# Performance work log

Measured on AMD Instinct MI355X. Metric: run time of the kernel, lower is better.

Reference implementation:

```python
import jax, jax.numpy as jnp
import numpy as np

EPS = 1e-5

def layernorm(x, w, b):
    mu = jnp.mean(x, axis=-1, keepdims=True)
    xc = x - mu
    var = jnp.mean(xc * xc, axis=-1, keepdims=True)
    return xc * jax.lax.rsqrt(var + EPS) * w + b

def setup_inputs() -> dict:
    key = jax.random.key(0)
    ks = jax.random.split(key, 9)
    B, T, Nm, Nl = 8, 8, 1024, 64
    Vw, Tw, H, Dh = 1024, 2048, 8, 64
    inner = H * Dh  # 512
    s_q = 1.0 / np.sqrt(Tw)
    s_kv = 1.0 / np.sqrt(Vw)
    s_o = 1.0 / np.sqrt(inner)
    return {
        "x": jax.random.normal(ks[0], (B, T, Nm, Vw), jnp.float32),
        "latents": jax.random.normal(ks[1], (B, T, Nl, Tw), jnp.float32),
        "nm_w": jnp.ones((Vw,), jnp.float32),
        "nm_b": jnp.zeros((Vw,), jnp.float32),
        "nl_w": jnp.ones((Tw,), jnp.float32),
        "nl_b": jnp.zeros((Tw,), jnp.float32),
        "Wq": jax.random.normal(ks[2], (Tw, inner), jnp.float32) * s_q,
        "Wkv": jax.random.normal(ks[3], (Vw, 2 * inner), jnp.float32) * s_kv,
        "Wout": jax.random.normal(ks[4], (inner, Tw), jnp.float32) * s_o,
    }

def reference(x, latents, nm_w, nm_b, nl_w, nl_b, Wq, Wkv, Wout):
    H, Dh = 8, 64
    scale = Dh ** (-0.5)
    B, T, Nm, _ = x.shape
    Nl = latents.shape[2]
    xn = layernorm(x, nm_w, nm_b)          # (B,T,Nm,Vw)
    ln = layernorm(latents, nl_w, nl_b)    # (B,T,Nl,Tw)
    q = (ln @ Wq).reshape(B, T, Nl, H, Dh)           # b t i h d
    kv = xn @ Wkv                                     # (B,T,Nm,2*inner)
    k, v = jnp.split(kv, 2, axis=-1)
    k = k.reshape(B, T, Nm, H, Dh)                    # b t j h d
    v = v.reshape(B, T, Nm, H, Dh)
    sim = jnp.einsum('btihd,btjhd->bthij', q * scale, k)  # (B,T,H,Nl,Nm)
    attn = jax.nn.softmax(sim, axis=-1)
    out = jnp.einsum('bthij,btjhd->btihd', attn, v)       # (B,T,Nl,H,Dh)
    out = out.reshape(B, T, Nl, H * Dh)
    return out @ Wout                                     # (B,T,Nl,Tw)
```

## Files before the change

kernel.cpp:

```cpp
#include <hip/hip_runtime.h>

typedef __attribute__((ext_vector_type(8))) short bfrag8;
typedef __attribute__((ext_vector_type(4))) float f32x4;

typedef const unsigned int __attribute__((address_space(1)))* gas1_u32;
typedef unsigned int __attribute__((address_space(3)))* gas3_u32;

#define DEV __device__ __forceinline__

DEV unsigned short f2bf(float f) {
  unsigned int u = __builtin_bit_cast(unsigned int, f);
  u += 0x7fffu + ((u >> 16) & 1u);
  return (unsigned short)(u >> 16);
}

DEV void gload_lds16(const void* g, void* l) {
  __builtin_amdgcn_global_load_lds((gas1_u32)g, (gas3_u32)l, 16, 0, 0);
}

__global__ __launch_bounds__(256) void k_xstats(
    const float* __restrict__ x, unsigned short* __restrict__ xb,
    float* __restrict__ mu, float* __restrict__ rstd)
{
  const int wid = threadIdx.x >> 6, lane = threadIdx.x & 63;
  const int row = blockIdx.x * 4 + wid;
  const float* base = x + (size_t)row * 1024;
  float4 v[4];
  #pragma unroll
  for (int i = 0; i < 4; ++i) v[i] = ((const float4*)base)[i * 64 + lane];
  float s = 0.f, q = 0.f;
  #pragma unroll
  for (int i = 0; i < 4; ++i) {
    s += v[i].x + v[i].y + v[i].z + v[i].w;
    q += v[i].x*v[i].x + v[i].y*v[i].y + v[i].z*v[i].z + v[i].w*v[i].w;
  }
  #pragma unroll
  for (int off = 32; off >= 1; off >>= 1) { s += __shfl_xor(s, off); q += __shfl_xor(q, off); }
  const float m  = s * (1.0f/1024.0f);
  const float var = q * (1.0f/1024.0f) - m * m;
  const float rs = rsqrtf(var + 1e-5f);
  if (lane == 0) { mu[row] = m; rstd[row] = rs; }
  unsigned short* ob = xb + (size_t)row * 1024;
  #pragma unroll
  for (int i = 0; i < 4; ++i) {
    ushort4 o;
    o.x = f2bf(v[i].x); o.y = f2bf(v[i].y); o.z = f2bf(v[i].z); o.w = f2bf(v[i].w);
    ((ushort4*)ob)[i * 64 + lane] = o;
  }
}

__global__ __launch_bounds__(256) void k_lnlat(
    const float* __restrict__ lat, const float* __restrict__ w,
    const float* __restrict__ b, unsigned short* __restrict__ ln)
{
  const int row = blockIdx.x, tid = threadIdx.x;
  const float* base = lat + (size_t)row * 2048;
  const float4 v0 = ((const float4*)base)[tid];
  const float4 v1 = ((const float4*)base)[256 + tid];
  float s = v0.x+v0.y+v0.z+v0.w + v1.x+v1.y+v1.z+v1.w;
  float q = v0.x*v0.x+v0.y*v0.y+v0.z*v0.z+v0.w*v0.w
          + v1.x*v1.x+v1.y*v1.y+v1.z*v1.z+v1.w*v1.w;
  #pragma unroll
  for (int off = 32; off >= 1; off >>= 1) { s += __shfl_xor(s, off); q += __shfl_xor(q, off); }
  __shared__ float red[8];
  const int wid = tid >> 6, lane = tid & 63;
  if (lane == 0) { red[wid] = s; red[4 + wid] = q; }
  __syncthreads();
  s = red[0] + red[1] + red[2] + red[3];
  q = red[4] + red[5] + red[6] + red[7];
  const float m  = s * (1.0f/2048.0f);
  const float var = q * (1.0f/2048.0f) - m * m;
  const float rs = rsqrtf(var + 1e-5f);
  const float4 w0 = ((const float4*)w)[tid], w1 = ((const float4*)w)[256 + tid];
  const float4 b0 = ((const float4*)b)[tid], b1 = ((const float4*)b)[256 + tid];
  ushort4 o0, o1;
  o0.x = f2bf((v0.x - m) * rs * w0.x + b0.x);
  o0.y = f2bf((v0.y - m) * rs * w0.y + b0.y);
  o0.z = f2bf((v0.z - m) * rs * w0.z + b0.z);
  o0.w = f2bf((v0.w - m) * rs * w0.w + b0.w);
  o1.x = f2bf((v1.x - m) * rs * w1.x + b1.x);
  o1.y = f2bf((v1.y - m) * rs * w1.y + b1.y);
  o1.z = f2bf((v1.z - m) * rs * w1.z + b1.z);
  o1.w = f2bf((v1.w - m) * rs * w1.w + b1.w);
  ((ushort4*)(ln + (size_t)row * 2048))[tid] = o0;
  ((ushort4*)(ln + (size_t)row * 2048))[256 + tid] = o1;
}

__global__ __launch_bounds__(256) void k_transpose_cast(
    const float* __restrict__ src, unsigned short* __restrict__ dst,
    int K, int N, const float* __restrict__ rowscale, float scale)
{
  __shared__ float tile[32][33];
  const int tx = threadIdx.x & 31, ty = threadIdx.x >> 5;
  const int ntiles = N >> 5;
  const int k0 = (blockIdx.x / ntiles) << 5;
  const int n0 = (blockIdx.x % ntiles) << 5;
  #pragma unroll
  for (int r = 0; r < 4; ++r) {
    const int kk = ty + r * 8;
    float v = src[(size_t)(k0 + kk) * N + n0 + tx] * scale;
    if (rowscale) v *= rowscale[k0 + kk];
    tile[kk][tx] = v;
  }
  __syncthreads();
  #pragma unroll
  for (int r = 0; r < 4; ++r) {
    const int nn = ty + r * 8;
    dst[(size_t)(n0 + nn) * K + k0 + tx] = f2bf(tile[tx][nn]);
  }
}

__global__ __launch_bounds__(256) void k_c1c2_part(
    const float* __restrict__ Wkv, const float* __restrict__ w,
    const float* __restrict__ b, float* __restrict__ part)
{
  const int kc = blockIdx.x;
  const int n  = blockIdx.y * 256 + threadIdx.x;
  float s1 = 0.f, s2 = 0.f;
  const int k0 = kc * 64;
  for (int k = k0; k < k0 + 64; ++k) {
    const float wv = Wkv[(size_t)k * 1024 + n];
    s1 += w[k] * wv;
    s2 += b[k] * wv;
  }
  part[(size_t)(kc * 2 + 0) * 1024 + n] = s1;
  part[(size_t)(kc * 2 + 1) * 1024 + n] = s2;
}

__global__ __launch_bounds__(256) void k_c1c2_red(
    const float* __restrict__ part, float* __restrict__ c1, float* __restrict__ c2)
{
  const int n = blockIdx.x * 256 + threadIdx.x;
  float s1 = 0.f, s2 = 0.f;
  #pragma unroll
  for (int kc = 0; kc < 16; ++kc) {
    s1 += part[(size_t)(kc * 2 + 0) * 1024 + n];
    s2 += part[(size_t)(kc * 2 + 1) * 1024 + n];
  }
  c1[n] = s1; c2[n] = s2;
}

template<int BM, int BN, int WM, int WN, int NT, int MODE>
__global__ __launch_bounds__(NT, 2) void k_gemm(
    const unsigned short* __restrict__ A, int lda,
    const unsigned short* __restrict__ Bt, int ldb,
    int K, int mtiles, int ntiles,
    void* __restrict__ Cout, int ldc,
    const float* __restrict__ mu, const float* __restrict__ rstd,
    const float* __restrict__ c1, const float* __restrict__ c2)
{
  constexpr int BK = 32;
  constexpr int NW = NT / 64;
  constexpr int MF = (BM / WM) / 16;
  constexpr int NF = (BN / WN) / 16;
  constexpr int LA = (BM * BK) / (8 * NT);
  constexpr int LB = (BN * BK) / (8 * NT);
  constexpr int RA = BM * BK;
  constexpr int RB = BN * BK;
  static_assert(WM * WN == NW, "wave grid");
  static_assert(LA >= 1 && LB >= 1, "tile too small for NT");

  __shared__ __attribute__((aligned(16))) unsigned short As[4 * RA];
  __shared__ __attribute__((aligned(16))) unsigned short Bs[4 * RB];

  int bid = blockIdx.x;
  {
    const int nwg = gridDim.x;
    if ((nwg & 7) == 0) {
      const int q = nwg >> 3;
      bid = (bid & 7) * q + (bid >> 3);
    }
  }
  const int mt = bid / ntiles, nt = bid % ntiles;
  const int tid = threadIdx.x;
  const int wid = tid >> 6, lane = tid & 63;
  const int g = lane >> 4, c = lane & 15;
  const int wr = wid / WN, wc = wid % WN;
  const int MO = wr * (BM / WM), NO = wc * (BN / WN);
  const int rot = (c >> 1) & 3;

  const unsigned short* gA = A + (size_t)mt * BM * lda;
  const unsigned short* gB = Bt + (size_t)nt * BN * ldb;

  const f32x4 zz = {0.f, 0.f, 0.f, 0.f};
  f32x4 acc[MF][NF];
  #pragma unroll
  for (int m = 0; m < MF; ++m)
    #pragma unroll
    for (int n = 0; n < NF; ++n) acc[m][n] = zz;

  auto stage = [&](int R, int kt) {
    #pragma unroll
    for (int i = 0; i < LA; ++i) {
      const int o = (i * NT + tid) * 16;
      const int row = o >> 6;
      const int slot = (o >> 4) & 3;
      const int srcb = (((slot - ((row >> 1) & 3)) & 3) << 4);
      gload_lds16((const char*)(gA + (size_t)row * lda + kt * BK) + srcb,
                  (char*)(As + R * RA) + o);
    }
    #pragma unroll
    for (int i = 0; i < LB; ++i) {
      const int o = (i * NT + tid) * 16;
      const int row = o >> 6;
      const int slot = (o >> 4) & 3;
      const int srcb = (((slot - ((row >> 1) & 3)) & 3) << 4);
      gload_lds16((const char*)(gB + (size_t)row * ldb + kt * BK) + srcb,
                  (char*)(Bs + R * RB) + o);
    }
  };

  auto compute = [&](int R) {
    const char* as = (const char*)(As + R * RA);
    const char* bs = (const char*)(Bs + R * RB);
    bfrag8 af[MF], bf[NF];
    #pragma unroll
    for (int m = 0; m < MF; ++m) {
      const int rw = MO + m * 16 + c;
      af[m] = *(const bfrag8*)(as + rw * 64 + (((g + rot) & 3) << 4));
    }
    #pragma unroll
    for (int n = 0; n < NF; ++n) {
      const int rw = NO + n * 16 + c;
      bf[n] = *(const bfrag8*)(bs + rw * 64 + (((g + rot) & 3) << 4));
    }
    #pragma unroll
    for (int m = 0; m < MF; ++m)
      #pragma unroll
      for (int n = 0; n < NF; ++n)
        acc[m][n] = __builtin_amdgcn_mfma_f32_16x16x32_bf16(af[m], bf[n], acc[m][n], 0, 0, 0);
  };

  const int nkt = K / BK;
  stage(0, 0); stage(1, 1); stage(2, 2);
  for (int t = 0; t < nkt; t += 4) {
    #pragma unroll
    for (int r = 0; r < 4; ++r) {
      int t3 = t + r + 3; if (t3 >= nkt) t3 -= nkt;
      asm volatile("s_waitcnt vmcnt(8)\n\ts_barrier" ::: "memory");
      stage((r + 3) & 3, t3);
      compute(r);
    }
  }

  #pragma unroll
  for (int m = 0; m < MF; ++m) {
    #pragma unroll
    for (int j = 0; j < 4; ++j) {
      const size_t orow = (size_t)mt * BM + MO + m * 16 + g * 4 + j;
      float rs = 0.f, muv = 0.f;
      if constexpr (MODE == 0) { rs = rstd[orow]; muv = mu[orow]; }
      #pragma unroll
      for (int n = 0; n < NF; ++n) {
        const int gcol = nt * BN + NO + n * 16 + c;
        float v = acc[m][n][j];
        if constexpr (MODE == 0) v = rs * (v - muv * c1[gcol]) + c2[gcol];
        if constexpr (MODE == 2) ((float*)Cout)[orow * ldc + gcol] = v;
        else ((unsigned short*)Cout)[orow * ldc + gcol] = f2bf(v);
      }
    }
  }
}

__global__ __launch_bounds__(256) void k_attn(
    const unsigned short* __restrict__ q,
    const unsigned short* __restrict__ kv,
    unsigned short* __restrict__ ao)
{
  __shared__ __attribute__((aligned(16))) unsigned short Vt[64 * 64];
  const int bid = blockIdx.x;
  const int bt = bid >> 3, h = bid & 7;
  const int tid = threadIdx.x;
  const int wid = tid >> 6, lane = tid & 63;
  const int g = lane >> 4, c = lane & 15;

  const size_t qoff = ((size_t)bt * 64 + wid * 16 + c) * 512 + h * 64;
  const bfrag8 qf0 = *(const bfrag8*)(q + qoff + g * 8);
  const bfrag8 qf1 = *(const bfrag8*)(q + qoff + 32 + g * 8);

  const f32x4 zz = {0.f, 0.f, 0.f, 0.f};
  f32x4 o[4] = {zz, zz, zz, zz};
  float m_run = -1e30f, l_run = 0.f;

  const size_t kvbase = (size_t)bt * 1024 * 1024;
  const unsigned short* kbase = kv + kvbase + h * 64;
  const unsigned short* vbase = kv + kvbase + 512 + h * 64;

  for (int ch = 0; ch < 16; ++ch) {
    #pragma unroll
    for (int rr = 0; rr < 2; ++rr) {
      const int key = rr * 32 + (tid >> 3);
      const int d0 = (tid & 7) * 8;
      const bfrag8 vv = *(const bfrag8*)(vbase + (size_t)(ch * 64 + key) * 1024 + d0);
      #pragma unroll
      for (int j = 0; j < 8; ++j)
        Vt[(d0 + j) * 64 + (key ^ (j << 3))] = (unsigned short)vv[j];
    }
    __syncthreads();
    #pragma unroll
    for (int ks = 0; ks < 2; ++ks) {
      const int kb = ch * 64 + ks * 32;
      f32x4 s[2];
      #pragma unroll
      for (int t = 0; t < 2; ++t) {
        const int kr = ((c >> 2) << 3) + (t << 2) + (c & 3);
        const unsigned short* krow = kbase + (size_t)(kb + kr) * 1024;
        s[t] = zz;
        s[t] = __builtin_amdgcn_mfma_f32_16x16x32_bf16(*(const bfrag8*)(krow + g * 8),      qf0, s[t], 0, 0, 0);
        s[t] = __builtin_amdgcn_mfma_f32_16x16x32_bf16(*(const bfrag8*)(krow + 32 + g * 8), qf1, s[t], 0, 0, 0);
      }
      float pm = s[0][0];
      #pragma unroll
      for (int i = 1; i < 4; ++i) pm = fmaxf(pm, s[0][i]);
      #pragma unroll
      for (int i = 0; i < 4; ++i) pm = fmaxf(pm, s[1][i]);
      pm = fmaxf(pm, __shfl_xor(pm, 16));
      pm = fmaxf(pm, __shfl_xor(pm, 32));
      const float mn = fmaxf(m_run, pm);
      const float alpha = __expf(m_run - mn);
      float p[8];
      #pragma unroll
      for (int i = 0; i < 4; ++i) p[i]     = __expf(s[0][i] - mn);
      #pragma unroll
      for (int i = 0; i < 4; ++i) p[4 + i] = __expf(s[1][i] - mn);
      float ts = 0.f;
      #pragma unroll
      for (int i = 0; i < 8; ++i) ts += p[i];
      ts += __shfl_xor(ts, 16);
      ts += __shfl_xor(ts, 32);
      l_run = l_run * alpha + ts;
      m_run = mn;
      float ar[4];
      #pragma unroll
      for (int rj = 0; rj < 4; ++rj) ar[rj] = __shfl(alpha, g * 4 + rj);
      #pragma unroll
      for (int db = 0; db < 4; ++db)
        #pragma unroll
        for (int j = 0; j < 4; ++j) o[db][j] *= ar[j];
      bfrag8 pa;
      #pragma unroll
      for (int i = 0; i < 8; ++i) pa[i] = (short)f2bf(p[i]);
      #pragma unroll
      for (int db = 0; db < 4; ++db) {
        const int d = db * 16 + c;
        const bfrag8 vb = *(const bfrag8*)(Vt + d * 64 + ((ks * 32 + g * 8) ^ ((c & 7) << 3)));
        o[db] = __builtin_amdgcn_mfma_f32_16x16x32_bf16(pa, vb, o[db], 0, 0, 0);
      }
    }
    __syncthreads();
  }
  float lr[4];
  #pragma unroll
  for (int rj = 0; rj < 4; ++rj) lr[rj] = __shfl(l_run, g * 4 + rj);
  #pragma unroll
  for (int db = 0; db < 4; ++db)
    #pragma unroll
    for (int j = 0; j < 4; ++j) {
      const float val = o[db][j] / lr[j];
      ao[((size_t)bt * 64 + wid * 16 + g * 4 + j) * 512 + h * 64 + db * 16 + c] = f2bf(val);
    }
}

extern "C" void kernel_launch(void* const* d_in, const int* in_sizes, int n_in,
                              void* d_out, int out_size, void* d_ws, size_t ws_size,
                              hipStream_t stream)
{
  const float* x    = (const float*)d_in[0];
  const float* lat  = (const float*)d_in[1];
  const float* nm_w = (const float*)d_in[2];
  const float* nm_b = (const float*)d_in[3];
  const float* nl_w = (const float*)d_in[4];
  const float* nl_b = (const float*)d_in[5];
  const float* Wq   = (const float*)d_in[6];
  const float* Wkv  = (const float*)d_in[7];
  const float* Wout = (const float*)d_in[8];

  char* p = (char*)d_ws;
  auto take = [&](size_t bytes) { char* r = p; p += (bytes + 255) & ~(size_t)255; return r; };
  unsigned short* xb    = (unsigned short*)take(64ull * 1024 * 1024 * 2);
  unsigned short* kvb   = (unsigned short*)take(64ull * 1024 * 1024 * 2);
  unsigned short* lnb   = (unsigned short*)take(4096ull * 2048 * 2);
  unsigned short* qbuf  = (unsigned short*)take(4096ull * 512 * 2);
  unsigned short* aob   = (unsigned short*)take(4096ull * 512 * 2);
  unsigned short* WqT   = (unsigned short*)take(512ull * 2048 * 2);
  unsigned short* WkvT  = (unsigned short*)take(1024ull * 1024 * 2);
  unsigned short* WoutT = (unsigned short*)take(2048ull * 512 * 2);
  float* muv  = (float*)take(65536ull * 4);
  float* rsd  = (float*)take(65536ull * 4);
  float* c1   = (float*)take(1024 * 4);
  float* c2   = (float*)take(1024 * 4);
  float* part = (float*)take(32ull * 1024 * 4);
  if ((size_t)(p - (char*)d_ws) > ws_size) return;

  k_transpose_cast<<<dim3(64 * 16), 256, 0, stream>>>(Wq,   WqT,   2048,  512, nullptr, 0.125f);
  k_transpose_cast<<<dim3(32 * 32), 256, 0, stream>>>(Wkv,  WkvT,  1024, 1024, nm_w,    1.0f);
  k_transpose_cast<<<dim3(16 * 64), 256, 0, stream>>>(Wout, WoutT,  512, 2048, nullptr, 1.0f);
  k_c1c2_part<<<dim3(16, 4), 256, 0, stream>>>(Wkv, nm_w, nm_b, part);
  k_c1c2_red<<<dim3(4), 256, 0, stream>>>(part, c1, c2);
  k_xstats<<<dim3(16384), 256, 0, stream>>>(x, xb, muv, rsd);
  k_lnlat<<<dim3(4096), 256, 0, stream>>>(lat, nl_w, nl_b, lnb);

  k_gemm<256, 256, 2, 4, 512, 0><<<dim3(1024), 512, 0, stream>>>(
      xb, 1024, WkvT, 1024, 1024, 256, 4, kvb, 1024, muv, rsd, c1, c2);
  k_gemm<128, 128, 2, 2, 256, 1><<<dim3(128), 256, 0, stream>>>(
      lnb, 2048, WqT, 2048, 2048, 32, 4, qbuf, 512, nullptr, nullptr, nullptr, nullptr);

  k_attn<<<dim3(512), 256, 0, stream>>>(qbuf, kvb, aob);

  k_gemm<128, 128, 2, 2, 256, 2><<<dim3(512), 256, 0, stream>>>(
      aob, 512, WoutT, 512, 512, 32, 16, d_out, 2048, nullptr, nullptr, nullptr, nullptr);
}
```

Baseline: 388.9 us.

## Add dedicated 8-wave KV GEMM with interleaved staging and retile Q/out GEMMs

Replaces the generic KV projection GEMM with a specialized 256x256 kernel using 64-wide K tiles, double-buffered 128KB LDS, and fine-grained interleaving of async global-to-LDS loads with MFMA blocks under s_setprio. The goal is to hide load latency behind matrix math and cut barrier stalls in the dominant GEMM. Separately, the Q and output GEMMs move to 64x128 tiles so they launch more workgroups, and the generic kernel's vmcnt gate now tracks its actual load count per stage. Risks include using a full 128KB of LDS, which limits occupancy, and hand-tuned wait counts that must match the issued loads exactly.

```diff
diff --git a/kernel.cpp b/kernel.cpp
--- a/kernel.cpp
+++ b/kernel.cpp
@@ -17,6 +17,11 @@
 DEV void gload_lds16(const void* g, void* l) {
   __builtin_amdgcn_global_load_lds((gas1_u32)g, (gas3_u32)l, 16, 0, 0);
 }
+
+template<int N> DEV void gate_bar();
+template<> DEV void gate_bar<4>() { asm volatile("s_waitcnt vmcnt(4)\n\ts_barrier" ::: "memory"); }
+template<> DEV void gate_bar<6>() { asm volatile("s_waitcnt vmcnt(6)\n\ts_barrier" ::: "memory"); }
+template<> DEV void gate_bar<8>() { asm volatile("s_waitcnt vmcnt(8)\n\ts_barrier" ::: "memory"); }
 
 __global__ __launch_bounds__(256) void k_xstats(
     const float* __restrict__ x, unsigned short* __restrict__ xb,
@@ -140,14 +145,156 @@
   c1[n] = s1; c2[n] = s2;
 }
 
+#define BAR8   __builtin_amdgcn_s_barrier()
+#define GATE4  do { gate_bar<4>(); __builtin_amdgcn_sched_barrier(0); } while (0)
+#define LGKM0  do { asm volatile("s_waitcnt lgkmcnt(0)" ::: "memory"); \
+                    __builtin_amdgcn_sched_barrier(0); } while (0)
+
+__global__ __launch_bounds__(512, 2) void k_gemm8(
+    const unsigned short* __restrict__ A,
+    const unsigned short* __restrict__ Bt,
+    unsigned short* __restrict__ C,
+    const float* __restrict__ mu, const float* __restrict__ rstd,
+    const float* __restrict__ c1, const float* __restrict__ c2)
+{
+  constexpr int NKT = 16;
+  __shared__ __attribute__((aligned(16))) char lds[131072];
+
+  int bid = blockIdx.x;
+  { const int nwg = gridDim.x; const int q = nwg >> 3; bid = (bid & 7) * q + (bid >> 3); }
+  const int mt = bid >> 2, nt = bid & 3;
+  const int tid = threadIdx.x;
+  const int wid = tid >> 6, lane = tid & 63;
+  const int g = lane >> 4, c = lane & 15;
+  const int wr = wid >> 2, wc = wid & 3;
+  const int MO = wr * 128, NO = wc * 64;
+
+  const unsigned short* gA = A + (size_t)mt * 256 * 1024;
+  const unsigned short* gB = Bt + (size_t)nt * 256 * 1024;
+
+  const f32x4 zz = {0.f, 0.f, 0.f, 0.f};
+  f32x4 acc[8][4];
+  #pragma unroll
+  for (int m = 0; m < 8; ++m)
+    #pragma unroll
+    for (int n = 0; n < 4; ++n) acc[m][n] = zz;
+
+  auto stageA = [&](int buf, int kk, int kt) {
+    #pragma unroll
+    for (int i = 0; i < 2; ++i) {
+      const int o = (i * 512 + tid) * 16;
+      const int row = o >> 6;
+      const int ss = ((((o >> 4) & 3) - (row >> 1)) & 3);
+      gload_lds16((const char*)(gA + (size_t)row * 1024 + kt * 64 + kk * 32) + ss * 16,
+                  lds + buf * 32768 + kk * 16384 + o);
+    }
+  };
+  auto stageB = [&](int buf, int kk, int kt) {
+    #pragma unroll
+    for (int i = 0; i < 2; ++i) {
+      const int o = (i * 512 + tid) * 16;
+      const int row = o >> 6;
+      const int ss = ((((o >> 4) & 3) - (row >> 1)) & 3);
+      gload_lds16((const char*)(gB + (size_t)row * 1024 + kt * 64 + kk * 32) + ss * 16,
+                  lds + 65536 + buf * 32768 + kk * 16384 + o);
+    }
+  };
+  auto rdA = [&](int buf, int kk, int m) -> bfrag8 {
+    const int row = MO + m * 16 + c;
+    return *(const bfrag8*)(lds + buf * 32768 + kk * 16384 + row * 64
+                            + (((g + (row >> 1)) & 3) << 4));
+  };
+  auto rdB = [&](int buf, int kk, int n) -> bfrag8 {
+    const int row = NO + n * 16 + c;
+    return *(const bfrag8*)(lds + 65536 + buf * 32768 + kk * 16384 + row * 64
+                            + (((g + (row >> 1)) & 3) << 4));
+  };
+
+  bfrag8 a[8], b0[4], b1[4];
+
+  auto tile4 = [&](int buf, int sb, int ukt) {
+    #pragma unroll
+    for (int m = 0; m < 8; ++m) a[m] = rdA(buf, 0, m);
+    #pragma unroll
+    for (int n = 0; n < 4; ++n) b0[n] = rdB(buf, 0, n);
+    stageA(sb, 0, ukt);
+    BAR8; LGKM0;
+    __builtin_amdgcn_s_setprio(1);
+    #pragma unroll
+    for (int m = 0; m < 8; ++m) {
+      acc[m][0] = __builtin_amdgcn_mfma_f32_16x16x32_bf16(a[m], b0[0], acc[m][0], 0, 0, 0);
+      acc[m][1] = __builtin_amdgcn_mfma_f32_16x16x32_bf16(a[m], b0[1], acc[m][1], 0, 0, 0);
+    }
+    __builtin_amdgcn_s_setprio(0);
+    GATE4;
+    #pragma unroll
+    for (int n = 0; n < 4; ++n) b1[n] = rdB(buf, 1, n);
+    stageB(sb, 0, ukt);
+    BAR8; LGKM0;
+    __builtin_amdgcn_s_setprio(1);
+    #pragma unroll
+    for (int m = 0; m < 8; ++m) {
+      acc[m][2] = __builtin_amdgcn_mfma_f32_16x16x32_bf16(a[m], b0[2], acc[m][2], 0, 0, 0);
+      acc[m][3] = __builtin_amdgcn_mfma_f32_16x16x32_bf16(a[m], b0[3], acc[m][3], 0, 0, 0);
+    }
+    __builtin_amdgcn_s_setprio(0);
+    GATE4;
+    #pragma unroll
+    for (int m = 0; m < 8; ++m) a[m] = rdA(buf, 1, m);
+    stageB(sb, 1, ukt);
+    BAR8; LGKM0;
+    __builtin_amdgcn_s_setprio(1);
+    #pragma unroll
+    for (int m = 0; m < 8; ++m) {
+      acc[m][0] = __builtin_amdgcn_mfma_f32_16x16x32_bf16(a[m], b1[0], acc[m][0], 0, 0, 0);
+      acc[m][1] = __builtin_amdgcn_mfma_f32_16x16x32_bf16(a[m], b1[1], acc[m][1], 0, 0, 0);
+    }
+    __builtin_amdgcn_s_setprio(0);
+    BAR8;
+    stageA(sb, 1, ukt);
+    BAR8; LGKM0;
+    __builtin_amdgcn_s_setprio(1);
+    #pragma unroll
+    for (int m = 0; m < 8; ++m) {
+      acc[m][2] = __builtin_amdgcn_mfma_f32_16x16x32_bf16(a[m], b1[2], acc[m][2], 0, 0, 0);
+      acc[m][3] = __builtin_amdgcn_mfma_f32_16x16x32_bf16(a[m], b1[3], acc[m][3], 0, 0, 0);
+    }
+    __builtin_amdgcn_s_setprio(0);
+    GATE4;
+  };
+
+  stageA(0, 0, 0); stageB(0, 0, 0); stageB(0, 1, 0); stageA(0, 1, 0);
+  GATE4;
+
+  for (int t = 0; t < NKT; t += 2) {
+    const int u2 = (t + 2 < NKT) ? t + 2 : 0;
+    tile4(0, 1, t + 1);
+    tile4(1, 0, u2);
+  }
+  asm volatile("s_waitcnt vmcnt(0)" ::: "memory");
+
+  #pragma unroll
+  for (int m = 0; m < 8; ++m) {
+    #pragma unroll
+    for (int j = 0; j < 4; ++j) {
+      const size_t orow = (size_t)mt * 256 + MO + m * 16 + g * 4 + j;
+      const float rs = rstd[orow], muv = mu[orow];
+      #pragma unroll
+      for (int n = 0; n < 4; ++n) {
+        const int gcol = nt * 256 + NO + n * 16 + c;
+        const float v = rs * (acc[m][n][j] - muv * c1[gcol]) + c2[gcol];
+        C[orow * 1024 + gcol] = f2bf(v);
+      }
+    }
+  }
+}
+
 template<int BM, int BN, int WM, int WN, int NT, int MODE>
 __global__ __launch_bounds__(NT, 2) void k_gemm(
     const unsigned short* __restrict__ A, int lda,
     const unsigned short* __restrict__ Bt, int ldb,
     int K, int mtiles, int ntiles,
-    void* __restrict__ Cout, int ldc,
-    const float* __restrict__ mu, const float* __restrict__ rstd,
-    const float* __restrict__ c1, const float* __restrict__ c2)
+    void* __restrict__ Cout, int ldc)
 {
   constexpr int BK = 32;
   constexpr int NW = NT / 64;
@@ -155,10 +302,12 @@
   constexpr int NF = (BN / WN) / 16;
   constexpr int LA = (BM * BK) / (8 * NT);
   constexpr int LB = (BN * BK) / (8 * NT);
+  constexpr int LPS = LA + LB;
   constexpr int RA = BM * BK;
   constexpr int RB = BN * BK;
   static_assert(WM * WN == NW, "wave grid");
   static_assert(LA >= 1 && LB >= 1, "tile too small for NT");
+  static_assert(LPS == 3 || LPS == 4, "gate specialization");
 
   __shared__ __attribute__((aligned(16))) unsigned short As[4 * RA];
   __shared__ __attribute__((aligned(16))) unsigned short Bs[4 * RB];
@@ -237,24 +386,23 @@
     #pragma unroll
     for (int r = 0; r < 4; ++r) {
       int t3 = t + r + 3; if (t3 >= nkt) t3 -= nkt;
-      asm volatile("s_waitcnt vmcnt(8)\n\ts_barrier" ::: "memory");
+      gate_bar<2 * LPS>();
+      __builtin_amdgcn_sched_barrier(0);
       stage((r + 3) & 3, t3);
       compute(r);
     }
   }
+  asm volatile("s_waitcnt vmcnt(0)" ::: "memory");
 
   #pragma unroll
   for (int m = 0; m < MF; ++m) {
     #pragma unroll
     for (int j = 0; j < 4; ++j) {
       const size_t orow = (size_t)mt * BM + MO + m * 16 + g * 4 + j;
-      float rs = 0.f, muv = 0.f;
-      if constexpr (MODE == 0) { rs = rstd[orow]; muv = mu[orow]; }
       #pragma unroll
       for (int n = 0; n < NF; ++n) {
         const int gcol = nt * BN + NO + n * 16 + c;
-        float v = acc[m][n][j];
-        if constexpr (MODE == 0) v = rs * (v - muv * c1[gcol]) + c2[gcol];
+        const float v = acc[m][n][j];
         if constexpr (MODE == 2) ((float*)Cout)[orow * ldc + gcol] = v;
         else ((unsigned short*)Cout)[orow * ldc + gcol] = f2bf(v);
       }
@@ -400,13 +548,12 @@
   k_xstats<<<dim3(16384), 256, 0, stream>>>(x, xb, muv, rsd);
   k_lnlat<<<dim3(4096), 256, 0, stream>>>(lat, nl_w, nl_b, lnb);
 
-  k_gemm<256, 256, 2, 4, 512, 0><<<dim3(1024), 512, 0, stream>>>(
-      xb, 1024, WkvT, 1024, 1024, 256, 4, kvb, 1024, muv, rsd, c1, c2);
-  k_gemm<128, 128, 2, 2, 256, 1><<<dim3(128), 256, 0, stream>>>(
-      lnb, 2048, WqT, 2048, 2048, 32, 4, qbuf, 512, nullptr, nullptr, nullptr, nullptr);
+  k_gemm8<<<dim3(1024), 512, 0, stream>>>(xb, WkvT, kvb, muv, rsd, c1, c2);
+  k_gemm<64, 128, 1, 4, 256, 1><<<dim3(256), 256, 0, stream>>>(
+      lnb, 2048, WqT, 2048, 2048, 64, 4, qbuf, 512);
 
   k_attn<<<dim3(512), 256, 0, stream>>>(qbuf, kvb, aob);
 
-  k_gemm<128, 128, 2, 2, 256, 2><<<dim3(512), 256, 0, stream>>>(
-      aob, 512, WoutT, 512, 512, 32, 16, d_out, 2048, nullptr, nullptr, nullptr, nullptr);
-}
+  k_gemm<64, 128, 1, 4, 256, 2><<<dim3(1024), 256, 0, stream>>>(
+      aob, 512, WoutT, 512, 512, 64, 16, d_out, 2048);
+}
```

New measurement: 378.4 us. 2.7% less time.

## Add dedicated KV GEMM kernel with register-held B fragments and retune other GEMMs

Applied to the files above, without the earlier changes.

Replaces the large 256x256 KV projection GEMM with a new 128x128 kernel. Only A tiles are staged through LDS, in a swizzled double buffer, while B fragments are loaded straight from global memory into registers and the LayerNorm correction is fused into the epilogue. The Q and output projections switch to 64x128 tiles to launch more workgroups, and the pipeline wait count is specialized per tile config. This trades LDS traffic and barrier cost for more global-load pressure and register use.

```diff
diff --git a/kernel.cpp b/kernel.cpp
--- a/kernel.cpp
+++ b/kernel.cpp
@@ -16,6 +16,12 @@
 
 DEV void gload_lds16(const void* g, void* l) {
   __builtin_amdgcn_global_load_lds((gas1_u32)g, (gas3_u32)l, 16, 0, 0);
+}
+
+template<int N> DEV void gate_bar();
+template<> DEV void gate_bar<6>() { asm volatile("s_waitcnt vmcnt(6)\n\ts_barrier" ::: "memory"); }
+template<> DEV void gate_bar<8>() {
+  asm volatile("s_waitcnt lgkmcnt(0)\n\ts_waitcnt vmcnt(8)\n\ts_barrier" ::: "memory");
 }
 
 __global__ __launch_bounds__(256) void k_xstats(
@@ -140,14 +146,114 @@
   c1[n] = s1; c2[n] = s2;
 }
 
+__global__ __launch_bounds__(256, 2) void k_gbr(
+    const unsigned short* __restrict__ A,
+    const unsigned short* __restrict__ Bt,
+    unsigned short* __restrict__ C,
+    const float* __restrict__ mu, const float* __restrict__ rstd,
+    const float* __restrict__ c1, const float* __restrict__ c2)
+{
+  constexpr int NKT = 16;
+  __shared__ __attribute__((aligned(16))) unsigned short Al[2][128 * 64];
+
+  int bid = blockIdx.x;
+  { const int nwg = gridDim.x; const int q = nwg >> 3; bid = (bid & 7) * q + (bid >> 3); }
+  const int mt = bid >> 3, nt = bid & 7;
+  const int tid = threadIdx.x;
+  const int wid = tid >> 6, lane = tid & 63;
+  const int g = lane >> 4, c = lane & 15;
+  const int wr = wid >> 1, wc = wid & 1;
+  const int MO = wr * 64, NO = wc * 64;
+
+  const unsigned short* gA = A + (size_t)mt * 128 * 1024;
+  const unsigned short* gB = Bt + (size_t)(nt * 128 + wc * 64 + c) * 1024;
+
+  const f32x4 zz = {0.f, 0.f, 0.f, 0.f};
+  f32x4 acc[4][4];
+  #pragma unroll
+  for (int m = 0; m < 4; ++m)
+    #pragma unroll
+    for (int n = 0; n < 4; ++n) acc[m][n] = zz;
+
+  auto stage = [&](int buf, int kt) {
+    #pragma unroll
+    for (int i = 0; i < 4; ++i) {
+      const int o = (i * 256 + tid) * 16;
+      const int r = o >> 7;
+      const int s = (o >> 4) & 7;
+      const int sg = (s - r) & 7;
+      gload_lds16((const char*)(gA + (size_t)r * 1024 + kt * 64) + sg * 16,
+                  (char*)&Al[buf][0] + o);
+    }
+  };
+  auto loadB = [&](bfrag8 (&b)[4][2], int kt) {
+    #pragma unroll
+    for (int nf = 0; nf < 4; ++nf)
+      #pragma unroll
+      for (int kk = 0; kk < 2; ++kk)
+        b[nf][kk] = *(const bfrag8*)(gB + (size_t)nf * 16 * 1024 + kt * 64 + kk * 32 + g * 8);
+  };
+  auto rdA = [&](int buf, int kk, int mf) -> bfrag8 {
+    const int r = MO + mf * 16 + c;
+    const int s = (kk * 4 + g + r) & 7;
+    return *(const bfrag8*)((const char*)&Al[buf][0] + r * 128 + s * 16);
+  };
+  auto compute = [&](int buf, const bfrag8 (&b)[4][2]) {
+    #pragma unroll
+    for (int kk = 0; kk < 2; ++kk) {
+      bfrag8 a[4];
+      #pragma unroll
+      for (int mf = 0; mf < 4; ++mf) a[mf] = rdA(buf, kk, mf);
+      #pragma unroll
+      for (int mf = 0; mf < 4; ++mf)
+        #pragma unroll
+        for (int nf = 0; nf < 4; ++nf)
+          acc[mf][nf] = __builtin_amdgcn_mfma_f32_16x16x32_bf16(a[mf], b[nf][kk], acc[mf][nf], 0, 0, 0);
+    }
+  };
+
+  bfrag8 bA[4][2], bB[4][2];
+
+  stage(0, 0);
+  loadB(bA, 0);
+  gate_bar<8>();
+
+  for (int t = 0; t < NKT; t += 2) {
+    const int u1 = t + 1;
+    const int u2 = (t + 2 < NKT) ? t + 2 : 0;
+    stage(1, u1);
+    loadB(bB, u1);
+    compute(0, bA);
+    gate_bar<8>();
+    stage(0, u2);
+    loadB(bA, u2);
+    compute(1, bB);
+    gate_bar<8>();
+  }
+  asm volatile("s_waitcnt vmcnt(0)" ::: "memory");
+
+  #pragma unroll
+  for (int m = 0; m < 4; ++m) {
+    #pragma unroll
+    for (int j = 0; j < 4; ++j) {
+      const size_t orow = (size_t)mt * 128 + MO + m * 16 + g * 4 + j;
+      const float rs = rstd[orow], muv = mu[orow];
+      #pragma unroll
+      for (int n = 0; n < 4; ++n) {
+        const int gcol = nt * 128 + NO + n * 16 + c;
+        const float v = rs * (acc[m][n][j] - muv * c1[gcol]) + c2[gcol];
+        C[orow * 1024 + gcol] = f2bf(v);
+      }
+    }
+  }
+}
+
 template<int BM, int BN, int WM, int WN, int NT, int MODE>
 __global__ __launch_bounds__(NT, 2) void k_gemm(
     const unsigned short* __restrict__ A, int lda,
     const unsigned short* __restrict__ Bt, int ldb,
     int K, int mtiles, int ntiles,
-    void* __restrict__ Cout, int ldc,
-    const float* __restrict__ mu, const float* __restrict__ rstd,
-    const float* __restrict__ c1, const float* __restrict__ c2)
+    void* __restrict__ Cout, int ldc)
 {
   constexpr int BK = 32;
   constexpr int NW = NT / 64;
@@ -155,10 +261,12 @@
   constexpr int NF = (BN / WN) / 16;
   constexpr int LA = (BM * BK) / (8 * NT);
   constexpr int LB = (BN * BK) / (8 * NT);
+  constexpr int LPS = LA + LB;
   constexpr int RA = BM * BK;
   constexpr int RB = BN * BK;
   static_assert(WM * WN == NW, "wave grid");
   static_assert(LA >= 1 && LB >= 1, "tile too small for NT");
+  static_assert(LPS == 3 || LPS == 4, "gate specialization");
 
   __shared__ __attribute__((aligned(16))) unsigned short As[4 * RA];
   __shared__ __attribute__((aligned(16))) unsigned short Bs[4 * RB];
@@ -237,24 +345,22 @@
     #pragma unroll
     for (int r = 0; r < 4; ++r) {
       int t3 = t + r + 3; if (t3 >= nkt) t3 -= nkt;
-      asm volatile("s_waitcnt vmcnt(8)\n\ts_barrier" ::: "memory");
+      gate_bar<2 * LPS>();
       stage((r + 3) & 3, t3);
       compute(r);
     }
   }
+  asm volatile("s_waitcnt vmcnt(0)" ::: "memory");
 
   #pragma unroll
   for (int m = 0; m < MF; ++m) {
     #pragma unroll
     for (int j = 0; j < 4; ++j) {
       const size_t orow = (size_t)mt * BM + MO + m * 16 + g * 4 + j;
-      float rs = 0.f, muv = 0.f;
-      if constexpr (MODE == 0) { rs = rstd[orow]; muv = mu[orow]; }
       #pragma unroll
       for (int n = 0; n < NF; ++n) {
         const int gcol = nt * BN + NO + n * 16 + c;
-        float v = acc[m][n][j];
-        if constexpr (MODE == 0) v = rs * (v - muv * c1[gcol]) + c2[gcol];
+        const float v = acc[m][n][j];
         if constexpr (MODE == 2) ((float*)Cout)[orow * ldc + gcol] = v;
         else ((unsigned short*)Cout)[orow * ldc + gcol] = f2bf(v);
       }
@@ -400,13 +506,12 @@
   k_xstats<<<dim3(16384), 256, 0, stream>>>(x, xb, muv, rsd);
   k_lnlat<<<dim3(4096), 256, 0, stream>>>(lat, nl_w, nl_b, lnb);
 
-  k_gemm<256, 256, 2, 4, 512, 0><<<dim3(1024), 512, 0, stream>>>(
-      xb, 1024, WkvT, 1024, 1024, 256, 4, kvb, 1024, muv, rsd, c1, c2);
-  k_gemm<128, 128, 2, 2, 256, 1><<<dim3(128), 256, 0, stream>>>(
-      lnb, 2048, WqT, 2048, 2048, 32, 4, qbuf, 512, nullptr, nullptr, nullptr, nullptr);
+  k_gbr<<<dim3(4096), 256, 0, stream>>>(xb, WkvT, kvb, muv, rsd, c1, c2);
+  k_gemm<64, 128, 1, 4, 256, 1><<<dim3(256), 256, 0, stream>>>(
+      lnb, 2048, WqT, 2048, 2048, 64, 4, qbuf, 512);
 
   k_attn<<<dim3(512), 256, 0, stream>>>(qbuf, kvb, aob);
 
-  k_gemm<128, 128, 2, 2, 256, 2><<<dim3(512), 256, 0, stream>>>(
-      aob, 512, WoutT, 512, 512, 32, 16, d_out, 2048, nullptr, nullptr, nullptr, nullptr);
-}
+  k_gemm<64, 128, 1, 4, 256, 2><<<dim3(1024), 256, 0, stream>>>(
+      aob, 512, WoutT, 512, 512, 64, 16, d_out, 2048);
+}
```

New measurement: 541.3 us. 1.39x slower.
